# Kernel tuning notes

Hardware: AMD Instinct MI355X
Metric: run time of the kernel (lower is better)

The kernel has to match this reference:

```python
import jax, jax.numpy as jnp
import numpy as np

N_DIM, D_SKETCH, M_COLS = 8192, 1024, 4096


def setup_inputs() -> dict:
    key = jax.random.key(0)
    kM, kD, kP = jax.random.split(key, 3)
    M = jax.random.normal(kM, (N_DIM, M_COLS), dtype=jnp.float32)
    # Rademacher signs, exactly as 2*(rand > 0.5).float() - 1
    D = 2.0 * (jax.random.uniform(kD, (N_DIM,)) > 0.5).astype(jnp.float32) - 1.0
    # np.random.choice(N, d) samples with replacement -> plain randint
    P = jax.random.randint(kP, (D_SKETCH,), 0, N_DIM)
    return {"M": M, "D": D, "P": P}


def _idct_rows(X, rows):
    # torch_dct.idct with norm=None along the last axis, evaluated only at the
    # output positions `rows` (identical values to full idct followed by gather):
    #   x[n] = (1/N) * ( X[...,0]/2 + sum_{k=1}^{N-1} X[...,k] * cos(pi*(2n+1)*k/(2N)) )
    N = X.shape[-1]
    k = jnp.arange(N, dtype=jnp.float32)
    w = jnp.where(k == 0, 0.5, 1.0) / N                      # DCT-III weights / N
    n = rows.astype(jnp.float32)
    ang = (jnp.pi / (2.0 * N)) * (2.0 * n[:, None] + 1.0) * k[None, :]
    C = jnp.cos(ang) * w[None, :]                            # [d, N]
    return jnp.einsum('dk,mk->md', C, X)                     # [m, d]


def reference(M, D, P):
    # SRFT sketch, 2-D branch, transpose=False:
    #   result = idct((D[:, None] * M).T).T[P, :]   ->  shape [d, m]
    X = D[:, None] * M                                       # sign flip, [N, m]
    out = _idct_rows(X.T, P)                                 # [m, d]
    return out.T                                             # [d, m]
```

## Files before the change

kernel.cpp:

```cpp
#include <hip/hip_runtime.h>

#define K_DIM 8192
#define M_OUT 1024
#define N_OUT 4096
#define BUFSZ 32768

typedef __attribute__((ext_vector_type(4))) float f32x4;
typedef __attribute__((ext_vector_type(8))) __bf16 bf16x8;
typedef __attribute__((ext_vector_type(2))) __bf16 bf16x2;
typedef __attribute__((ext_vector_type(8))) unsigned short u16x8;

__device__ __forceinline__ unsigned short f2bf(float x) {
  unsigned u = __builtin_bit_cast(unsigned, x);
  u += 0x7fffu + ((u >> 16) & 1u);
  return (unsigned short)(u >> 16);
}

__device__ __forceinline__ unsigned pack2(float a, float b) {
  bf16x2 v;
  v[0] = (__bf16)a;
  v[1] = (__bf16)b;
  return __builtin_bit_cast(unsigned, v);
}

__global__ __launch_bounds__(256) void build_c_kernel(
    const int* __restrict__ Pp, const float* __restrict__ Dp,
    unsigned short* __restrict__ Cm) {
  const int p = blockIdx.x;
  const int n2 = 2 * Pp[p] + 1;
  const int t = threadIdx.x;
#pragma unroll
  for (int ch = 0; ch < 4; ++ch) {
    const int kb = (ch << 11) + (t << 3);
    u16x8 o;
#pragma unroll
    for (int i = 0; i < 8; ++i) {
      const int k = kb + i;
      const unsigned tt = ((unsigned)(n2 * k)) & 32767u;
      const float cv = cosf((float)tt * 1.9174759848570515e-4f);
      const float wk = (k == 0) ? (0.5f / 8192.0f) : (1.0f / 8192.0f);
      o[i] = f2bf(cv * wk * Dp[k]);
    }
    *(u16x8*)(Cm + ((size_t)p << 13) + kb) = o;
  }
}

__global__ __launch_bounds__(512, 4) void gemm_kernel(
    const unsigned short* __restrict__ Cm, const float* __restrict__ Mp,
    float* __restrict__ outp, int kchunk, int nwg, int ksplit) {
  __shared__ __align__(16) char lds[2 * BUFSZ];

  const int id = blockIdx.x;
  const int chunk = nwg >> 3;
  const int sid = (id & 7) * chunk + (id >> 3);
  const int bz = sid % ksplit;
  const int rest = sid / ksplit;
  const int bm = rest & 7, bn = rest >> 3;

  const int t = threadIdx.x;
  const int w = t >> 6, l = t & 63;
  const int wr = w >> 2, wc = w & 3;
  const int lg = l >> 4, lr = l & 15;
  const int k_begin = bz * kchunk;
  const int NT = kchunk >> 6;

  const int arow = t >> 3;
  const int acol = ((t & 7) << 4) ^ ((arow & 7) << 4);
  const char* Agl = (const char*)Cm + ((size_t)(bm * 128 + arow) << 14) +
                    ((size_t)k_begin << 1) + acol;
  auto stageA = [&](int nbuf, int tile) {
    char* d = (char*)lds + nbuf * BUFSZ + t * 16;
    const char* s = Agl + ((size_t)tile << 7);
#pragma unroll
    for (int i = 0; i < 2; ++i)
      __builtin_amdgcn_global_load_lds(
          (const __attribute__((address_space(1))) void*)(s + ((size_t)i << 20)),
          (__attribute__((address_space(3))) void*)(d + i * 8192), 16, 0, 0);
  };

  const int bk0 = w * 8 + (l >> 5) * 4;
  const int bn0 = (l & 31) * 4;
  const float* Bg = Mp + (size_t)k_begin * N_OUT + bn * 128 + bn0;
  auto loadB = [&](f32x4 (&r)[4], int tile) {
#pragma unroll
    for (int i = 0; i < 4; ++i)
      r[i] = *(const f32x4*)(Bg + (size_t)(tile * 64 + bk0 + i) * N_OUT);
  };
  auto writeB = [&](const f32x4 (&r)[4], int nbuf) {
#pragma unroll
    for (int nn = 0; nn < 4; ++nn) {
      const int n = bn0 + nn;
      const int sN = (n & 7) ^ ((n >> 2) & 7);
      uint2 pk;
      pk.x = pack2(r[0][nn], r[1][nn]);
      pk.y = pack2(r[2][nn], r[3][nn]);
      *(uint2*)(lds + nbuf * BUFSZ + 16384 + n * 128 + ((w ^ sN) << 4) +
                ((l >> 5) << 3)) = pk;
    }
  };

  const int sw = (lr & 7) << 4;
  const int xk0 = (lg << 4) ^ sw;
  const int xk1 = (64 + (lg << 4)) ^ sw;
  unsigned boff[2][2];
#pragma unroll
  for (int kk = 0; kk < 2; ++kk)
#pragma unroll
    for (int nf = 0; nf < 2; ++nf) {
      const int row = wc * 32 + nf * 16 + lr;
      const int sN = (row & 7) ^ ((row >> 2) & 7);
      boff[kk][nf] = 16384 + row * 128 + ((((kk << 2) | lg) ^ sN) << 4);
    }

  f32x4 acc[4][2] = {};
  bf16x8 Af[4];
  bf16x8 Bf[2];

  auto readA = [&](int nbuf, int xk) {
    const char* aBuf = (const char*)lds + nbuf * BUFSZ + wr * 8192 + lr * 128;
#pragma unroll
    for (int m = 0; m < 4; ++m)
      Af[m] = *(const bf16x8*)(aBuf + m * 2048 + xk);
  };
  auto readB = [&](int nbuf, int kk) {
#pragma unroll
    for (int nf = 0; nf < 2; ++nf)
      Bf[nf] = *(const bf16x8*)(lds + nbuf * BUFSZ + boff[kk][nf]);
  };
  auto mm = [&]() {
    __builtin_amdgcn_s_setprio(1);
#pragma unroll
    for (int m = 0; m < 4; ++m)
#pragma unroll
      for (int nf = 0; nf < 2; ++nf)
        acc[m][nf] = __builtin_amdgcn_mfma_f32_16x16x32_bf16(
            Af[m], Bf[nf], acc[m][nf], 0, 0, 0);
    __builtin_amdgcn_s_setprio(0);
  };

  {
    f32x4 p0[4];
    stageA(0, 0);
    loadB(p0, 0);
    writeB(p0, 0);
    asm volatile("s_waitcnt vmcnt(0) lgkmcnt(0)" ::: "memory");
    __builtin_amdgcn_sched_barrier(0);
    __builtin_amdgcn_s_barrier();
  }

  for (int tt = 0; tt < NT; ++tt) {
    const int cur = tt & 1, nxt = cur ^ 1;
    const bool more = (tt + 1) < NT;
    f32x4 sb[4];
    if (more) {
      loadB(sb, tt + 1);
      stageA(nxt, tt + 1);
    }
    readB(cur, 0);
    readA(cur, xk0);
    mm();
    if (more) writeB(sb, nxt);
    readB(cur, 1);
    readA(cur, xk1);
    mm();
    asm volatile("s_waitcnt vmcnt(0) lgkmcnt(0)" ::: "memory");
    __builtin_amdgcn_sched_barrier(0);
    __builtin_amdgcn_s_barrier();
  }

  float* po = outp + (size_t)bz * (M_OUT * N_OUT);
  const int orow = bm * 128 + wr * 64;
  const int ocol = bn * 128 + wc * 32 + lr;
#pragma unroll
  for (int m = 0; m < 4; ++m) {
    const int r0 = orow + m * 16 + (lg << 2);
#pragma unroll
    for (int nf = 0; nf < 2; ++nf) {
      const int c = ocol + nf * 16;
#pragma unroll
      for (int q = 0; q < 4; ++q)
        po[(size_t)(r0 + q) * N_OUT + c] = acc[m][nf][q];
    }
  }
}

__global__ __launch_bounds__(256) void reduce_kernel(
    const float* __restrict__ part, float* __restrict__ out, int ksplit) {
  const size_t total = (size_t)M_OUT * N_OUT;
  const size_t i = ((size_t)blockIdx.x * 256 + threadIdx.x) * 4;
  if (i >= total) return;
  f32x4 s = *(const f32x4*)(part + i);
  for (int s2 = 1; s2 < ksplit; ++s2) s += *(const f32x4*)(part + (size_t)s2 * total + i);
  *(f32x4*)(out + i) = s;
}

__global__ __launch_bounds__(256) void naive_kernel(
    const float* __restrict__ Mp, const float* __restrict__ Dp,
    const int* __restrict__ Pp, float* __restrict__ out) {
  const int p = blockIdx.y;
  const int j = blockIdx.x * 256 + threadIdx.x;
  const int n2 = 2 * Pp[p] + 1;
  float acc = 0.0f;
  for (int k = 0; k < K_DIM; ++k) {
    const unsigned tt = ((unsigned)(n2 * k)) & 32767u;
    const float cv = cosf((float)tt * 1.9174759848570515e-4f);
    const float wk = (k == 0) ? 0.5f : 1.0f;
    acc += cv * wk * Dp[k] * Mp[(size_t)k * N_OUT + j];
  }
  out[(size_t)p * N_OUT + j] = acc * (1.0f / 8192.0f);
}

extern "C" void kernel_launch(void* const* d_in, const int* in_sizes, int n_in,
                              void* d_out, int out_size, void* d_ws, size_t ws_size,
                              hipStream_t stream) {
  const float* Mp = (const float*)d_in[0];
  const float* Dp = (const float*)d_in[1];
  const int* Pp = (const int*)d_in[2];
  float* out = (float*)d_out;

  const size_t CM_BYTES = (size_t)M_OUT * K_DIM * 2;
  const size_t PART_BYTES = (size_t)M_OUT * N_OUT * 4;

  int ksplit;
  if (ws_size >= CM_BYTES + 2 * PART_BYTES) ksplit = 2;
  else if (ws_size >= CM_BYTES) ksplit = 1;
  else ksplit = 0;

  if (ksplit == 0) {
    naive_kernel<<<dim3(N_OUT / 256, M_OUT), 256, 0, stream>>>(Mp, Dp, Pp, out);
    return;
  }

  unsigned short* Cm = (unsigned short*)d_ws;
  float* part = (float*)((char*)d_ws + CM_BYTES);

  build_c_kernel<<<dim3(M_OUT), 256, 0, stream>>>(Pp, Dp, Cm);

  float* gout = (ksplit > 1) ? part : out;
  const int kchunk = K_DIM / ksplit;
  const int nwg = (M_OUT / 128) * (N_OUT / 128) * ksplit;
  gemm_kernel<<<dim3(nwg), 512, 0, stream>>>(Cm, Mp, gout, kchunk, nwg, ksplit);

  if (ksplit > 1)
    reduce_kernel<<<dim3((M_OUT * N_OUT / 4 + 255) / 256), 256, 0, stream>>>(part, out, ksplit);
}
```

Before: 118.9 us.

## Use 4 waves per tile with 64x64 per-wave output in GEMM

Halves the GEMM workgroup to 256 threads, with each wave computing a 64x64 sub-tile (4x4 MFMA fragments) instead of 64x32, raising fragment reuse from LDS. Staging loads per thread double to cover the same 128x128x64 tile, and the priority hints around the MFMA block are removed. The split-K index mapping is now hardcoded to a two-way split, which trades fewer waves for latency hiding against lower LDS read traffic per FLOP.

```diff
diff --git a/kernel.cpp b/kernel.cpp
--- a/kernel.cpp
+++ b/kernel.cpp
@@ -8,6 +8,7 @@
 typedef __attribute__((ext_vector_type(4))) float f32x4;
 typedef __attribute__((ext_vector_type(8))) __bf16 bf16x8;
 typedef __attribute__((ext_vector_type(2))) __bf16 bf16x2;
+typedef __attribute__((ext_vector_type(4))) unsigned u32x4;
 typedef __attribute__((ext_vector_type(8))) unsigned short u16x8;
 
 __device__ __forceinline__ unsigned short f2bf(float x) {
@@ -45,21 +46,19 @@
   }
 }
 
-__global__ __launch_bounds__(512, 4) void gemm_kernel(
+__global__ __launch_bounds__(256, 2) void gemm_kernel(
     const unsigned short* __restrict__ Cm, const float* __restrict__ Mp,
-    float* __restrict__ outp, int kchunk, int nwg, int ksplit) {
+    float* __restrict__ outp, int kchunk, int nwg) {
   __shared__ __align__(16) char lds[2 * BUFSZ];
 
   const int id = blockIdx.x;
   const int chunk = nwg >> 3;
   const int sid = (id & 7) * chunk + (id >> 3);
-  const int bz = sid % ksplit;
-  const int rest = sid / ksplit;
-  const int bm = rest & 7, bn = rest >> 3;
+  const int bz = sid & 1, bm = (sid >> 1) & 7, bn = sid >> 4;
 
   const int t = threadIdx.x;
   const int w = t >> 6, l = t & 63;
-  const int wr = w >> 2, wc = w & 3;
+  const int wr = w >> 1, wc = w & 1;
   const int lg = l >> 4, lr = l & 15;
   const int k_begin = bz * kchunk;
   const int NT = kchunk >> 6;
@@ -72,49 +71,49 @@
     char* d = (char*)lds + nbuf * BUFSZ + t * 16;
     const char* s = Agl + ((size_t)tile << 7);
 #pragma unroll
-    for (int i = 0; i < 2; ++i)
+    for (int i = 0; i < 4; ++i)
       __builtin_amdgcn_global_load_lds(
-          (const __attribute__((address_space(1))) void*)(s + ((size_t)i << 20)),
-          (__attribute__((address_space(3))) void*)(d + i * 8192), 16, 0, 0);
-  };
-
-  const int bk0 = w * 8 + (l >> 5) * 4;
-  const int bn0 = (l & 31) * 4;
+          (const __attribute__((address_space(1))) void*)(s + ((size_t)i << 19)),
+          (__attribute__((address_space(3))) void*)(d + i * 4096), 16, 0, 0);
+  };
+
+  const int bk0 = (t >> 5) * 8;
+  const int bn0 = (t & 31) * 4;
   const float* Bg = Mp + (size_t)k_begin * N_OUT + bn * 128 + bn0;
-  auto loadB = [&](f32x4 (&r)[4], int tile) {
-#pragma unroll
-    for (int i = 0; i < 4; ++i)
+  auto loadB = [&](f32x4 (&r)[8], int tile) {
+#pragma unroll
+    for (int i = 0; i < 8; ++i)
       r[i] = *(const f32x4*)(Bg + (size_t)(tile * 64 + bk0 + i) * N_OUT);
   };
-  auto writeB = [&](const f32x4 (&r)[4], int nbuf) {
+  auto writeB = [&](const f32x4 (&r)[8], int nbuf) {
 #pragma unroll
     for (int nn = 0; nn < 4; ++nn) {
       const int n = bn0 + nn;
       const int sN = (n & 7) ^ ((n >> 2) & 7);
-      uint2 pk;
-      pk.x = pack2(r[0][nn], r[1][nn]);
-      pk.y = pack2(r[2][nn], r[3][nn]);
-      *(uint2*)(lds + nbuf * BUFSZ + 16384 + n * 128 + ((w ^ sN) << 4) +
-                ((l >> 5) << 3)) = pk;
+      u32x4 pk;
+#pragma unroll
+      for (int j = 0; j < 4; ++j) pk[j] = pack2(r[2 * j][nn], r[2 * j + 1][nn]);
+      *(u32x4*)(lds + nbuf * BUFSZ + 16384 + n * 128 +
+                (((t >> 5) ^ sN) << 4)) = pk;
     }
   };
 
   const int sw = (lr & 7) << 4;
   const int xk0 = (lg << 4) ^ sw;
   const int xk1 = (64 + (lg << 4)) ^ sw;
-  unsigned boff[2][2];
+  unsigned boff[2][4];
 #pragma unroll
   for (int kk = 0; kk < 2; ++kk)
 #pragma unroll
-    for (int nf = 0; nf < 2; ++nf) {
-      const int row = wc * 32 + nf * 16 + lr;
+    for (int nf = 0; nf < 4; ++nf) {
+      const int row = wc * 64 + nf * 16 + lr;
       const int sN = (row & 7) ^ ((row >> 2) & 7);
       boff[kk][nf] = 16384 + row * 128 + ((((kk << 2) | lg) ^ sN) << 4);
     }
 
-  f32x4 acc[4][2] = {};
+  f32x4 acc[4][4] = {};
   bf16x8 Af[4];
-  bf16x8 Bf[2];
+  bf16x8 Bf[4];
 
   auto readA = [&](int nbuf, int xk) {
     const char* aBuf = (const char*)lds + nbuf * BUFSZ + wr * 8192 + lr * 128;
@@ -124,25 +123,23 @@
   };
   auto readB = [&](int nbuf, int kk) {
 #pragma unroll
-    for (int nf = 0; nf < 2; ++nf)
+    for (int nf = 0; nf < 4; ++nf)
       Bf[nf] = *(const bf16x8*)(lds + nbuf * BUFSZ + boff[kk][nf]);
   };
   auto mm = [&]() {
-    __builtin_amdgcn_s_setprio(1);
 #pragma unroll
     for (int m = 0; m < 4; ++m)
 #pragma unroll
-      for (int nf = 0; nf < 2; ++nf)
+      for (int nf = 0; nf < 4; ++nf)
         acc[m][nf] = __builtin_amdgcn_mfma_f32_16x16x32_bf16(
             Af[m], Bf[nf], acc[m][nf], 0, 0, 0);
-    __builtin_amdgcn_s_setprio(0);
   };
 
   {
-    f32x4 p0[4];
+    f32x4 p[8];
     stageA(0, 0);
-    loadB(p0, 0);
-    writeB(p0, 0);
+    loadB(p, 0);
+    writeB(p, 0);
     asm volatile("s_waitcnt vmcnt(0) lgkmcnt(0)" ::: "memory");
     __builtin_amdgcn_sched_barrier(0);
     __builtin_amdgcn_s_barrier();
@@ -151,7 +148,7 @@
   for (int tt = 0; tt < NT; ++tt) {
     const int cur = tt & 1, nxt = cur ^ 1;
     const bool more = (tt + 1) < NT;
-    f32x4 sb[4];
+    f32x4 sb[8];
     if (more) {
       loadB(sb, tt + 1);
       stageA(nxt, tt + 1);
@@ -170,12 +167,12 @@
 
   float* po = outp + (size_t)bz * (M_OUT * N_OUT);
   const int orow = bm * 128 + wr * 64;
-  const int ocol = bn * 128 + wc * 32 + lr;
+  const int ocol = bn * 128 + wc * 64 + lr;
 #pragma unroll
   for (int m = 0; m < 4; ++m) {
     const int r0 = orow + m * 16 + (lg << 2);
 #pragma unroll
-    for (int nf = 0; nf < 2; ++nf) {
+    for (int nf = 0; nf < 4; ++nf) {
       const int c = ocol + nf * 16;
 #pragma unroll
       for (int q = 0; q < 4; ++q)
@@ -239,7 +236,7 @@
   float* gout = (ksplit > 1) ? part : out;
   const int kchunk = K_DIM / ksplit;
   const int nwg = (M_OUT / 128) * (N_OUT / 128) * ksplit;
-  gemm_kernel<<<dim3(nwg), 512, 0, stream>>>(Cm, Mp, gout, kchunk, nwg, ksplit);
+  gemm_kernel<<<dim3(nwg), 256, 0, stream>>>(Cm, Mp, gout, kchunk, nwg);
 
   if (ksplit > 1)
     reduce_kernel<<<dim3((M_OUT * N_OUT / 4 + 255) / 256), 256, 0, stream>>>(part, out, ksplit);
```

Measured after the change: 118.2 us. Within noise of the previous version (-0.5%).
